# Performance work log

Hardware: AMD Instinct MI355X
Metric: run time of the kernel (lower is better)

Reference implementation:

```python
import jax, jax.numpy as jnp
import numpy as np
from functools import partial
from jax import lax

K = 3
CIN = 64
COUT = 128
D = 4
H_STEP = 1.0
EPS = 1e-8
SCALE = 1.0


@partial(jax.custom_vjp, nondiff_argnums=(1,))
def spike_fn(x, scale):
    # SurrogateHeaviside forward: hard step
    return (x > 0).astype(x.dtype)


def _spike_fwd(x, scale):
    return spike_fn(x, scale), x


def _spike_bwd(scale, x, g):
    # surrogate gradient: derivative of sigmoid(scale * x)
    sig = jax.nn.sigmoid(scale * x)
    return (g * scale * sig * (1.0 - sig),)


spike_fn.defvjp(_spike_fwd, _spike_bwd)


def setup_inputs() -> dict:
    key = jax.random.key(0)
    k1, k2, k3, k4 = jax.random.split(key, 4)
    x = jax.random.normal(k1, (32, CIN, 64, 64), dtype=jnp.float32)
    mem = jnp.zeros((32, COUT, 64, 64), dtype=jnp.float32)
    # ME kernel layout: [K*K, Cin, Cout]; xavier-ish scale
    kernel = jax.random.normal(k2, (K * K, CIN, COUT), dtype=jnp.float32) * 0.05
    beta = 0.8 + 0.01 * jax.random.normal(k3, (1,), dtype=jnp.float32)
    b = 0.1 + 0.01 * jax.random.normal(k4, (COUT,), dtype=jnp.float32)
    return {"x": x, "mem": mem, "kernel": kernel, "beta": beta, "b": b, "bs": 32}


def reference(x, mem, kernel, beta, b, bs):
    # sparse conv densified -> plain strided conv on dense input
    w = kernel.reshape(K, K, CIN, COUT).transpose(3, 2, 0, 1)  # OIHW
    conv_dense = lax.conv_general_dilated(
        x, w, window_strides=(1, 1), padding="SAME",
        dimension_numbers=("NCHW", "OIHW", "NCHW"))  # [bs, Cout, H, W]

    # LIF membrane update
    new_mem = mem * beta + conv_dense * (1.0 - beta)

    # per-out-channel kernel norm scaling, minus threshold bias
    norm = jnp.sum(kernel ** 2, axis=(0, 1))  # [Cout]
    mthr = new_mem / (norm + EPS)[None, :, None, None] - b[None, :, None, None]

    # multi-threshold spike count
    spk = jnp.zeros_like(mthr)
    for d in range(D):
        spk = spk + spike_fn(mthr - d * H_STEP, SCALE)

    spk_mask = (spk > 0).astype(new_mem.dtype)
    final_mem = new_mem * (1.0 - spk_mask)
    return spk, final_mem
```

## Files before the change

### kernel.cpp

```cpp
#include <hip/hip_runtime.h>


typedef _Float16 half8 __attribute__((ext_vector_type(8)));
typedef float f32x4 __attribute__((ext_vector_type(4)));

constexpr int CIc = 64, COc = 128, HHc = 64, WWc = 64, NBc = 32;
constexpr float EPSB = 5e-5f;
constexpr unsigned CAPc = 1u << 18;

constexpr size_t O_CNT   = 0;
constexpr size_t O_NORMD = 16;
constexpr size_t O_RNORM = O_NORMD + 1024;
constexpr size_t O_WDT   = O_RNORM + 512;
constexpr size_t O_WHI   = O_WDT + 589824;
constexpr size_t O_WLO   = O_WHI + 147456;
constexpr size_t O_LIST  = O_WLO + 147456;
constexpr size_t WS_NEED = O_LIST + (size_t)CAPc * 4;

__global__ void prep_kernel(const float* __restrict__ w, double* __restrict__ normd,
                            float* __restrict__ rnormf, double* __restrict__ wdT,
                            _Float16* __restrict__ whi, _Float16* __restrict__ wlo,
                            unsigned* __restrict__ counter) {
    const int bx = blockIdx.x;
    if (bx < 128) {
        const int co = bx, lane = threadIdx.x & 63;
        if (threadIdx.x >= 64) return;
        double s = 0.0;
        #pragma unroll
        for (int k = 0; k < 9; ++k) {
            const double v = (double)w[(k * 64 + lane) * COc + co];
            s = fma(v, v, s);
        }
        #pragma unroll
        for (int off = 32; off; off >>= 1) s += __shfl_xor(s, off);
        if (lane == 0) {
            s += 1e-8;
            normd[co]  = s;
            rnormf[co] = (float)(1.0 / s);
            if (co == 0) counter[0] = 0u;
        }
    } else {
        const int i = (bx - 128) * 256 + threadIdx.x;
        if (i >= 9 * CIc * COc) return;
        const int ci = i & 63, t = (i >> 6) % 9, co = i / (9 * 64);
        const float v = w[(t * CIc + ci) * COc + co];
        wdT[i] = (double)v;
        if (whi) {
            const int i2 = (t * COc + co) * CIc + ci;
            const _Float16 h = (_Float16)v;
            whi[i2] = h;
            wlo[i2] = (_Float16)(v - (float)h);
        }
    }
}

__global__ __launch_bounds__(256, 2) void convM(
    const float* __restrict__ x,
    const float* __restrict__ mem,
    const _Float16* __restrict__ whi,
    const _Float16* __restrict__ wlo,
    const float* __restrict__ beta_p,
    const float* __restrict__ bias,
    const float* __restrict__ rnormf,
    float* __restrict__ out_spk, float* __restrict__ out_mem,
    unsigned* __restrict__ counter, unsigned* __restrict__ list)
{
    __shared__ half8 xs[4224];
    char* xsb = (char*)(&xs[0]);

    const int tid = threadIdx.x;
    const int y0 = blockIdx.x * 8;
    const int cohalf = blockIdx.y;
    const int n = blockIdx.z;

    const int lane   = tid & 63;
    const int wv     = tid >> 6;
    const int co0    = cohalf * 64 + wv * 16;
    const int lanelo = lane & 15;
    const int kgi    = (lane >> 4) * 8;
    const unsigned kg2 = (unsigned)(lane >> 4) * 16;

    half8 wH[9][2], wL[9][2];
    {
        const int co = co0 + lanelo;
        const _Float16* wh = whi + (size_t)co * CIc + kgi;
        const _Float16* wl = wlo + (size_t)co * CIc + kgi;
        #pragma unroll
        for (int t = 0; t < 9; ++t)
            #pragma unroll
            for (int cs = 0; cs < 2; ++cs) {
                wH[t][cs] = *(const half8*)(wh + (size_t)t * COc * CIc + cs * 32);
                wL[t][cs] = *(const half8*)(wl + (size_t)t * COc * CIc + cs * 32);
            }
    }

    float xr[3][8];

    auto issueRow = [&](int rabs) {
        #pragma unroll
        for (int c = 0; c < 3; ++c) {
            const int it = tid + c * 256;
            if (it < 528) {
                const int px1 = it % 66, cig = it / 66;
                const int px = px1 - 1;
                const bool val = ((unsigned)px < 64u) && ((unsigned)rabs < 64u);
                const float* xp = x + (((size_t)n * CIc + cig * 8) * HHc
                                       + (val ? rabs : 0)) * WWc + (val ? px : 0);
                #pragma unroll
                for (int j2 = 0; j2 < 8; ++j2)
                    xr[c][j2] = val ? xp[j2 * (HHc * WWc)] : 0.0f;
            }
        }
    };
    auto writeRow = [&](int rabs) {
        const int slot = (rabs + 8) & 3;
        char* sb = xsb + slot * 16896;
        #pragma unroll
        for (int c = 0; c < 3; ++c) {
            const int it = tid + c * 256;
            if (it < 528) {
                const int px1 = it % 66, cig = it / 66;
                half8 hv, lv;
                #pragma unroll
                for (int j2 = 0; j2 < 8; ++j2) {
                    const float f = xr[c][j2];
                    const _Float16 h = (_Float16)f;
                    hv[j2] = h;
                    lv[j2] = (_Float16)(f - (float)h);
                }
                const unsigned off = (unsigned)px1 * 128
                                   + (((unsigned)cig * 16) ^ (((unsigned)px1 & 7) << 4));
                *(half8*)(sb + off)        = hv;
                *(half8*)(sb + 8448 + off) = lv;
            }
        }
    };

    issueRow(y0 - 1); writeRow(y0 - 1);
    issueRow(y0);     writeRow(y0);
    issueRow(y0 + 1); writeRow(y0 + 1);
    issueRow(y0 + 2);
    asm volatile("s_waitcnt lgkmcnt(0)" ::: "memory");
    __builtin_amdgcn_s_barrier();

    const float beta = beta_p[0];
    const float omb  = 1.0f - beta;
    float rnv[4], biv[4];
    #pragma unroll
    for (int r = 0; r < 4; ++r) {
        const int co = co0 + (lane >> 4) * 4 + r;
        rnv[r] = rnormf[co];
        biv[r] = bias[co];
    }

    for (int j = 0; j < 8; ++j) {
        const int y = y0 + j;

        if (j < 7) writeRow(y + 2);
        if (j < 6) issueRow(y + 3);

        float mv[4][4];
        #pragma unroll
        for (int r = 0; r < 4; ++r) {
            const int co = co0 + (lane >> 4) * 4 + r;
            const float* mp = mem + (((size_t)n * COc + co) * HHc + y) * WWc + lanelo;
            #pragma unroll
            for (int pf = 0; pf < 4; ++pf) mv[r][pf] = mp[pf * 16];
        }

        f32x4 acc[4];
        #pragma unroll
        for (int pf = 0; pf < 4; ++pf) acc[pf] = f32x4{0.f, 0.f, 0.f, 0.f};

        __builtin_amdgcn_s_setprio(1);
        #pragma unroll
        for (int t = 0; t < 9; ++t) {
            const int dy = t / 3, dx = t % 3;
            const unsigned sbase = (unsigned)((y - 1 + dy + 8) & 3) * 16896;
            #pragma unroll
            for (int cs = 0; cs < 2; ++cs) {
                #pragma unroll
                for (int pf = 0; pf < 4; ++pf) {
                    const int px1 = pf * 16 + lanelo + dx;
                    const unsigned ob = sbase + (unsigned)px1 * 128
                        + (((unsigned)(cs * 64) + kg2) ^ (((unsigned)px1 & 7) << 4));
                    const half8 bh = *(const half8*)(xsb + ob);
                    const half8 bl = *(const half8*)(xsb + 8448 + ob);
                    acc[pf] = __builtin_amdgcn_mfma_f32_16x16x32_f16(wH[t][cs], bh, acc[pf], 0, 0, 0);
                    acc[pf] = __builtin_amdgcn_mfma_f32_16x16x32_f16(wH[t][cs], bl, acc[pf], 0, 0, 0);
                    acc[pf] = __builtin_amdgcn_mfma_f32_16x16x32_f16(wL[t][cs], bh, acc[pf], 0, 0, 0);
                }
            }
        }
        __builtin_amdgcn_s_setprio(0);

        unsigned flm = 0u;
        #pragma unroll
        for (int pf = 0; pf < 4; ++pf) {
            const int px = pf * 16 + lanelo;
            #pragma unroll
            for (int r = 0; r < 4; ++r) {
                const int co = co0 + (lane >> 4) * 4 + r;
                const size_t idx = (((size_t)n * COc + co) * HHc + y) * WWc + px;
                const float nm   = fmaf(mv[r][pf], beta, acc[pf][r] * omb);
                const float mthr = fmaf(nm, rnv[r], -biv[r]);
                const float cm = fminf(fmaxf(ceilf(mthr), 0.0f), 4.0f);
                out_spk[idx] = cm;
                out_mem[idx] = (cm > 0.0f) ? 0.0f : nm;
                const float fr = rintf(mthr);
                const bool fl = (fabsf(mthr - fr) < EPSB) &
                                (fr >= 0.0f) & (fr <= 3.5f);
                flm |= ((unsigned)fl) << (pf * 4 + r);
            }
        }
        if (__ballot(flm != 0u)) {
            #pragma unroll
            for (int pf = 0; pf < 4; ++pf) {
                #pragma unroll
                for (int r = 0; r < 4; ++r) {
                    const unsigned long long msk =
                        __ballot((flm >> (pf * 4 + r)) & 1u);
                    if (msk) {
                        unsigned wb = 0;
                        if (lane == 0)
                            wb = atomicAdd(counter, (unsigned)__popcll(msk));
                        wb = __shfl(wb, 0);
                        if ((flm >> (pf * 4 + r)) & 1u) {
                            const int px = pf * 16 + lanelo;
                            const int co = co0 + (lane >> 4) * 4 + r;
                            const size_t idx =
                                (((size_t)n * COc + co) * HHc + y) * WWc + px;
                            const unsigned pos = wb +
                                (unsigned)__popcll(msk & ((1ull << lane) - 1ull));
                            if (pos < CAPc) list[pos] = (unsigned)idx;
                        }
                    }
                }
            }
        }

        asm volatile("s_waitcnt lgkmcnt(0)" ::: "memory");
        __builtin_amdgcn_s_barrier();
    }
}

__global__ __launch_bounds__(256) void fixB(
    const float* __restrict__ x, const float* __restrict__ mem,
    const float* __restrict__ beta_p, const float* __restrict__ bias,
    const double* __restrict__ normd, const double* __restrict__ wdT,
    const unsigned* __restrict__ counter, const unsigned* __restrict__ list,
    float* __restrict__ out_spk, float* __restrict__ out_mem)
{
    const int lane  = threadIdx.x & 63;
    const int wave  = blockIdx.x * 4 + (threadIdx.x >> 6);
    const int nwave = gridDim.x * 4;
    const unsigned cnt = min(counter[0], CAPc);
    const double beta = (double)beta_p[0];
    const double omb  = 1.0 - beta;

    for (unsigned p = wave; p < cnt; p += nwave) {
        const unsigned idx = list[p];
        const int xp = idx & 63, yp = (idx >> 6) & 63;
        const int co = (idx >> 12) & 127, n = idx >> 19;

        const float*  xc = x + ((size_t)n * CIc + lane) * (HHc * WWc);
        const double* wt = wdT + (size_t)co * 9 * CIc + lane;

        double a = 0.0;
        #pragma unroll
        for (int t = 0; t < 9; ++t) {
            const int yy = yp + t / 3 - 1, xx = xp + t % 3 - 1;
            const bool v = ((unsigned)yy < 64u) && ((unsigned)xx < 64u);
            const int yyc = min(max(yy, 0), 63), xxc = min(max(xx, 0), 63);
            const double xv = v ? (double)xc[yyc * WWc + xxc] : 0.0;
            a = fma(xv, wt[t * CIc], a);
        }
        #pragma unroll
        for (int off = 32; off; off >>= 1) a += __shfl_xor(a, off);

        if (lane == 0) {
            const double nm   = (double)mem[idx] * beta + a * omb;
            const double mthr = nm / normd[co] - (double)bias[co];
            const int s = (mthr > 0.) + (mthr > 1.) + (mthr > 2.) + (mthr > 3.);
            out_spk[idx] = (float)s;
            out_mem[idx] = (s > 0) ? 0.0f : (float)nm;
        }
    }
}

__global__ __launch_bounds__(256) void conv_fp64_fb(
    const float* __restrict__ x, const float* __restrict__ mem,
    const float* __restrict__ w, const float* __restrict__ beta_p,
    const float* __restrict__ bias, const double* __restrict__ normd,
    float* __restrict__ out_spk, float* __restrict__ out_mem)
{
    const int ix = threadIdx.x, iy = blockIdx.x * 4 + threadIdx.y;
    const int co0 = blockIdx.y * 8, n = blockIdx.z;
    bool valid[9]; int xoff[9];
    #pragma unroll
    for (int kh = 0; kh < 3; ++kh) {
        const int yy = iy + kh - 1;
        #pragma unroll
        for (int kw = 0; kw < 3; ++kw) {
            const int xx = ix + kw - 1, t = kh * 3 + kw;
            valid[t] = ((unsigned)yy < 64u) && ((unsigned)xx < 64u);
            xoff[t]  = yy * WWc + xx;
        }
    }
    double acc[8];
    #pragma unroll
    for (int j = 0; j < 8; ++j) acc[j] = 0.0;
    const float* xb = x + (size_t)n * CIc * HHc * WWc;
    for (int ci = 0; ci < CIc; ++ci) {
        const float* xc = xb + (size_t)ci * HHc * WWc;
        #pragma unroll
        for (int t = 0; t < 9; ++t) {
            const double xv = valid[t] ? (double)xc[xoff[t]] : 0.0;
            const float* wt = w + ((size_t)t * CIc + ci) * COc + co0;
            #pragma unroll
            for (int j = 0; j < 8; ++j) acc[j] = fma(xv, (double)wt[j], acc[j]);
        }
    }
    const double beta = (double)beta_p[0], omb = 1.0 - beta;
    const size_t base = (((size_t)n * COc + co0) * HHc + iy) * WWc + ix;
    #pragma unroll
    for (int j = 0; j < 8; ++j) {
        const size_t idx = base + (size_t)j * (HHc * WWc);
        const double nm   = (double)mem[idx] * beta + acc[j] * omb;
        const double mthr = nm / normd[co0 + j] - (double)bias[co0 + j];
        const int s = (mthr > 0.) + (mthr > 1.) + (mthr > 2.) + (mthr > 3.);
        out_spk[idx] = (float)s;
        out_mem[idx] = (s > 0) ? 0.0f : (float)nm;
    }
}

extern "C" void kernel_launch(void* const* d_in, const int* in_sizes, int n_in,
                              void* d_out, int out_size, void* d_ws, size_t ws_size,
                              hipStream_t stream) {
    const float* x      = (const float*)d_in[0];
    const float* mem    = (const float*)d_in[1];
    const float* w      = (const float*)d_in[2];
    const float* beta_p = (const float*)d_in[3];
    const float* bias   = (const float*)d_in[4];

    float* out_spk = (float*)d_out;
    float* out_mem = out_spk + (size_t)NBc * COc * HHc * WWc;

    char* ws = (char*)d_ws;
    unsigned* counter = (unsigned*)(ws + O_CNT);
    double*   normd   = (double*)(ws + O_NORMD);
    float*    rnormf  = (float*)(ws + O_RNORM);
    double*   wdT     = (double*)(ws + O_WDT);
    _Float16* whi     = (_Float16*)(ws + O_WHI);
    _Float16* wlo     = (_Float16*)(ws + O_WLO);
    unsigned* list    = (unsigned*)(ws + O_LIST);

    if (ws_size >= WS_NEED) {
        prep_kernel<<<128 + 288, 256, 0, stream>>>(w, normd, rnormf, wdT, whi, wlo,
                                                   counter);
        dim3 grdM(8, 2, NBc);
        convM<<<grdM, 256, 0, stream>>>(x, mem, whi, wlo, beta_p, bias, rnormf,
                                        out_spk, out_mem, counter, list);
        fixB<<<512, 256, 0, stream>>>(x, mem, beta_p, bias, normd, wdT,
                                      counter, list, out_spk, out_mem);
    } else {
        prep_kernel<<<128, 256, 0, stream>>>(w, normd, rnormf, wdT, nullptr, nullptr,
                                             counter);
        dim3 blk(WWc, 4, 1);
        dim3 grd(HHc / 4, COc / 8, NBc);
        conv_fp64_fb<<<grd, blk, 0, stream>>>(x, mem, w, beta_p, bias, normd,
                                              out_spk, out_mem);
    }
}
```

Baseline: 354.4 us.

## Drop fp16 hi/lo split to single fp16 MFMA, widen fix-up band, halve rows per block

Measured after the change: 523.5 us. 1.48x slower.

```diff
diff --git a/kernel.cpp b/kernel.cpp
--- a/kernel.cpp
+++ b/kernel.cpp
@@ -5,7 +5,7 @@
 typedef float f32x4 __attribute__((ext_vector_type(4)));
 
 constexpr int CIc = 64, COc = 128, HHc = 64, WWc = 64, NBc = 32;
-constexpr float EPSB = 5e-5f;
+constexpr float EPSB = 2e-4f;
 constexpr unsigned CAPc = 1u << 18;
 
 constexpr size_t O_CNT   = 0;
@@ -13,14 +13,12 @@
 constexpr size_t O_RNORM = O_NORMD + 1024;
 constexpr size_t O_WDT   = O_RNORM + 512;
 constexpr size_t O_WHI   = O_WDT + 589824;
-constexpr size_t O_WLO   = O_WHI + 147456;
-constexpr size_t O_LIST  = O_WLO + 147456;
+constexpr size_t O_LIST  = O_WHI + 147456;
 constexpr size_t WS_NEED = O_LIST + (size_t)CAPc * 4;
 
 __global__ void prep_kernel(const float* __restrict__ w, double* __restrict__ normd,
                             float* __restrict__ rnormf, double* __restrict__ wdT,
-                            _Float16* __restrict__ whi, _Float16* __restrict__ wlo,
-                            unsigned* __restrict__ counter) {
+                            _Float16* __restrict__ whi, unsigned* __restrict__ counter) {
     const int bx = blockIdx.x;
     if (bx < 128) {
         const int co = bx, lane = threadIdx.x & 63;
@@ -47,29 +45,26 @@
         wdT[i] = (double)v;
         if (whi) {
             const int i2 = (t * COc + co) * CIc + ci;
-            const _Float16 h = (_Float16)v;
-            whi[i2] = h;
-            wlo[i2] = (_Float16)(v - (float)h);
-        }
-    }
-}
-
-__global__ __launch_bounds__(256, 2) void convM(
+            whi[i2] = (_Float16)v;
+        }
+    }
+}
+
+__global__ __launch_bounds__(256, 4) void convM(
     const float* __restrict__ x,
     const float* __restrict__ mem,
     const _Float16* __restrict__ whi,
-    const _Float16* __restrict__ wlo,
     const float* __restrict__ beta_p,
     const float* __restrict__ bias,
     const float* __restrict__ rnormf,
     float* __restrict__ out_spk, float* __restrict__ out_mem,
     unsigned* __restrict__ counter, unsigned* __restrict__ list)
 {
-    __shared__ half8 xs[4224];
+    __shared__ half8 xs[2112];
     char* xsb = (char*)(&xs[0]);
 
     const int tid = threadIdx.x;
-    const int y0 = blockIdx.x * 8;
+    const int y0 = blockIdx.x * 4;
     const int cohalf = blockIdx.y;
     const int n = blockIdx.z;
 
@@ -80,18 +75,15 @@
     const int kgi    = (lane >> 4) * 8;
     const unsigned kg2 = (unsigned)(lane >> 4) * 16;
 
-    half8 wH[9][2], wL[9][2];
+    half8 wH[9][2];
     {
         const int co = co0 + lanelo;
         const _Float16* wh = whi + (size_t)co * CIc + kgi;
-        const _Float16* wl = wlo + (size_t)co * CIc + kgi;
         #pragma unroll
         for (int t = 0; t < 9; ++t)
             #pragma unroll
-            for (int cs = 0; cs < 2; ++cs) {
+            for (int cs = 0; cs < 2; ++cs)
                 wH[t][cs] = *(const half8*)(wh + (size_t)t * COc * CIc + cs * 32);
-                wL[t][cs] = *(const half8*)(wl + (size_t)t * COc * CIc + cs * 32);
-            }
     }
 
     float xr[3][8];
@@ -114,24 +106,19 @@
     };
     auto writeRow = [&](int rabs) {
         const int slot = (rabs + 8) & 3;
-        char* sb = xsb + slot * 16896;
+        char* sb = xsb + slot * 8448;
         #pragma unroll
         for (int c = 0; c < 3; ++c) {
             const int it = tid + c * 256;
             if (it < 528) {
                 const int px1 = it % 66, cig = it / 66;
-                half8 hv, lv;
+                half8 hv;
                 #pragma unroll
-                for (int j2 = 0; j2 < 8; ++j2) {
-                    const float f = xr[c][j2];
-                    const _Float16 h = (_Float16)f;
-                    hv[j2] = h;
-                    lv[j2] = (_Float16)(f - (float)h);
-                }
+                for (int j2 = 0; j2 < 8; ++j2)
+                    hv[j2] = (_Float16)xr[c][j2];
                 const unsigned off = (unsigned)px1 * 128
                                    + (((unsigned)cig * 16) ^ (((unsigned)px1 & 7) << 4));
-                *(half8*)(sb + off)        = hv;
-                *(half8*)(sb + 8448 + off) = lv;
+                *(half8*)(sb + off) = hv;
             }
         }
     };
@@ -153,20 +140,10 @@
         biv[r] = bias[co];
     }
 
-    for (int j = 0; j < 8; ++j) {
+    for (int j = 0; j < 4; ++j) {
         const int y = y0 + j;
 
-        if (j < 7) writeRow(y + 2);
-        if (j < 6) issueRow(y + 3);
-
-        float mv[4][4];
-        #pragma unroll
-        for (int r = 0; r < 4; ++r) {
-            const int co = co0 + (lane >> 4) * 4 + r;
-            const float* mp = mem + (((size_t)n * COc + co) * HHc + y) * WWc + lanelo;
-            #pragma unroll
-            for (int pf = 0; pf < 4; ++pf) mv[r][pf] = mp[pf * 16];
-        }
+        if (j < 3) writeRow(y + 2);
 
         f32x4 acc[4];
         #pragma unroll
@@ -176,7 +153,7 @@
         #pragma unroll
         for (int t = 0; t < 9; ++t) {
             const int dy = t / 3, dx = t % 3;
-            const unsigned sbase = (unsigned)((y - 1 + dy + 8) & 3) * 16896;
+            const unsigned sbase = (unsigned)((y - 1 + dy + 8) & 3) * 8448;
             #pragma unroll
             for (int cs = 0; cs < 2; ++cs) {
                 #pragma unroll
@@ -185,10 +162,7 @@
                     const unsigned ob = sbase + (unsigned)px1 * 128
                         + (((unsigned)(cs * 64) + kg2) ^ (((unsigned)px1 & 7) << 4));
                     const half8 bh = *(const half8*)(xsb + ob);
-                    const half8 bl = *(const half8*)(xsb + 8448 + ob);
                     acc[pf] = __builtin_amdgcn_mfma_f32_16x16x32_f16(wH[t][cs], bh, acc[pf], 0, 0, 0);
-                    acc[pf] = __builtin_amdgcn_mfma_f32_16x16x32_f16(wH[t][cs], bl, acc[pf], 0, 0, 0);
-                    acc[pf] = __builtin_amdgcn_mfma_f32_16x16x32_f16(wL[t][cs], bh, acc[pf], 0, 0, 0);
                 }
             }
         }
@@ -202,7 +176,7 @@
             for (int r = 0; r < 4; ++r) {
                 const int co = co0 + (lane >> 4) * 4 + r;
                 const size_t idx = (((size_t)n * COc + co) * HHc + y) * WWc + px;
-                const float nm   = fmaf(mv[r][pf], beta, acc[pf][r] * omb);
+                const float nm   = fmaf(mem[idx], beta, acc[pf][r] * omb);
                 const float mthr = fmaf(nm, rnv[r], -biv[r]);
                 const float cm = fminf(fmaxf(ceilf(mthr), 0.0f), 4.0f);
                 out_spk[idx] = cm;
@@ -239,6 +213,8 @@
             }
         }
 
+        if (j < 2) issueRow(y + 3);
+
         asm volatile("s_waitcnt lgkmcnt(0)" ::: "memory");
         __builtin_amdgcn_s_barrier();
     }
@@ -352,19 +328,18 @@
     float*    rnormf  = (float*)(ws + O_RNORM);
     double*   wdT     = (double*)(ws + O_WDT);
     _Float16* whi     = (_Float16*)(ws + O_WHI);
-    _Float16* wlo     = (_Float16*)(ws + O_WLO);
     unsigned* list    = (unsigned*)(ws + O_LIST);
 
     if (ws_size >= WS_NEED) {
-        prep_kernel<<<128 + 288, 256, 0, stream>>>(w, normd, rnormf, wdT, whi, wlo,
+        prep_kernel<<<128 + 288, 256, 0, stream>>>(w, normd, rnormf, wdT, whi,
                                                    counter);
-        dim3 grdM(8, 2, NBc);
-        convM<<<grdM, 256, 0, stream>>>(x, mem, whi, wlo, beta_p, bias, rnormf,
+        dim3 grdM(16, 2, NBc);
+        convM<<<grdM, 256, 0, stream>>>(x, mem, whi, beta_p, bias, rnormf,
                                         out_spk, out_mem, counter, list);
         fixB<<<512, 256, 0, stream>>>(x, mem, beta_p, bias, normd, wdT,
                                       counter, list, out_spk, out_mem);
     } else {
-        prep_kernel<<<128, 256, 0, stream>>>(w, normd, rnormf, wdT, nullptr, nullptr,
+        prep_kernel<<<128, 256, 0, stream>>>(w, normd, rnormf, wdT, nullptr,
                                              counter);
         dim3 blk(WWc, 4, 1);
         dim3 grd(HHc / 4, COc / 8, NBc);
```
